# Kernel optimization log

Hardware: AMD Instinct MI355X
Metric: run time of the kernel (lower is better)

The kernel has to match this reference:

```python
import jax, jax.numpy as jnp
import numpy as np

N = 100000
IN_DIM = 128
HIDDEN = 128
HEADS = 8
NUM_CLASSES = 64
NEG_SLOPE = 0.2
LN_EPS = 1e-5


def _glorot(key, shape):
    fan_in, fan_out = shape[0], shape[-1]
    lim = jnp.sqrt(6.0 / (fan_in + fan_out))
    return jax.random.uniform(key, shape, jnp.float32, -lim, lim)


def setup_inputs() -> dict:
    key = jax.random.key(0)
    ks = jax.random.split(key, 12)
    x = jax.random.normal(ks[0], (N, IN_DIM), jnp.float32)
    edge_index = jax.random.randint(ks[1], (2, 1600000), 0, N, jnp.int32)
    C1 = HIDDEN // HEADS
    return {
        "x": x,
        "edge_index": edge_index,
        # GATConv 1: in_dim -> heads * (hidden/heads), concat=True
        "W1": _glorot(ks[2], (IN_DIM, HEADS * C1)),
        "att_src1": _glorot(ks[3], (HEADS, C1)),
        "att_dst1": _glorot(ks[4], (HEADS, C1)),
        "bias1": jnp.zeros((HEADS * C1,), jnp.float32),
        # residual linear (no bias)
        "res_W": _glorot(ks[5], (IN_DIM, HIDDEN)),
        # LayerNorm
        "gamma": jnp.ones((HIDDEN,), jnp.float32),
        "beta": jnp.zeros((HIDDEN,), jnp.float32),
        # GATConv 2: hidden -> num_classes, heads=1, concat=False
        "W2": _glorot(ks[6], (HIDDEN, NUM_CLASSES)),
        "att_src2": _glorot(ks[7], (1, NUM_CLASSES)),
        "att_dst2": _glorot(ks[8], (1, NUM_CLASSES)),
        "bias2": jnp.zeros((NUM_CLASSES,), jnp.float32),
    }


def gat_conv(x, src, dst, W, att_src, att_dst, bias, heads, concat):
    n = x.shape[0]
    h = (x @ W).reshape(n, heads, -1)                     # [N,H,C]
    a_src = (h * att_src).sum(-1)                         # [N,H]
    a_dst = (h * att_dst).sum(-1)                         # [N,H]
    e = jax.nn.leaky_relu(a_src[src] + a_dst[dst], NEG_SLOPE)  # [E,H]
    # softmax over incoming edges of each destination node
    m = jax.ops.segment_max(e, dst, num_segments=n)
    m = jnp.where(jnp.isfinite(m), m, 0.0)
    e = jnp.exp(e - m[dst])
    s = jax.ops.segment_sum(e, dst, num_segments=n)
    alpha = e / (s[dst] + 1e-16)                          # [E,H]
    msg = h[src] * alpha[:, :, None]                      # [E,H,C]
    out = jax.ops.segment_sum(msg, dst, num_segments=n)   # [N,H,C]
    out = out.reshape(n, -1) if concat else out.mean(axis=1)
    return out + bias


def layer_norm(h, gamma, beta):
    mu = h.mean(-1, keepdims=True)
    var = ((h - mu) ** 2).mean(-1, keepdims=True)
    return (h - mu) * jax.lax.rsqrt(var + LN_EPS) * gamma + beta


def reference(x, edge_index, W1, att_src1, att_dst1, bias1, res_W,
              gamma, beta, W2, att_src2, att_dst2, bias2):
    n = x.shape[0]
    # PyG GATConv adds self-loops by default
    loop = jnp.arange(n, dtype=edge_index.dtype)
    src = jnp.concatenate([edge_index[0], loop])
    dst = jnp.concatenate([edge_index[1], loop])
    # eval mode: all dropouts are identity
    h = gat_conv(x, src, dst, W1, att_src1, att_dst1, bias1, HEADS, True)
    h = h + x @ res_W
    h = layer_norm(h, gamma, beta)
    h = jax.nn.elu(h)
    logits = gat_conv(h, src, dst, W2, att_src2, att_dst2, bias2, 1, False)
    return (h, logits)
```

## Files before the change

kernel.cpp:

```cpp
#include <hip/hip_runtime.h>
#include <hip/hip_bf16.h>

typedef __attribute__((ext_vector_type(8))) short bf16x8;
typedef __attribute__((ext_vector_type(4))) float f32x4;

__device__ __forceinline__ float bfu(unsigned short u){
  union{ unsigned int i; float f; } c; c.i = ((unsigned)u) << 16; return c.f;
}
__device__ __forceinline__ float bflo(unsigned u){
  union{ unsigned int i; float f; } c; c.i = u << 16; return c.f;
}
__device__ __forceinline__ float bfhi(unsigned u){
  union{ unsigned int i; float f; } c; c.i = u & 0xffff0000u; return c.f;
}
__device__ __forceinline__ float ldval(const void* p, int i, int f32){
  return f32 ? ((const float*)p)[i] : bfu(((const unsigned short*)p)[i]);
}
__device__ __forceinline__ bf16x8 packbf8(float4 u, float4 v){
  union { bf16x8 v8; __hip_bfloat16 h[8]; } r;
  r.h[0]=__float2bfloat16(u.x); r.h[1]=__float2bfloat16(u.y);
  r.h[2]=__float2bfloat16(u.z); r.h[3]=__float2bfloat16(u.w);
  r.h[4]=__float2bfloat16(v.x); r.h[5]=__float2bfloat16(v.y);
  r.h[6]=__float2bfloat16(v.z); r.h[7]=__float2bfloat16(v.w);
  return r.v8;
}
__device__ __forceinline__ float lrelu(float v){ return v > 0.f ? v : 0.2f*v; }

__global__ void detect(const unsigned short* __restrict__ xh, int* __restrict__ flag){
  int i = blockIdx.x*256 + threadIdx.x;
  float v = fabsf(bfu(xh[i]));
  if (v > 1e4f) atomicOr(flag, 1);
}

__global__ void prep(const void* W1, const void* resW, const void* W2,
                     const void* a1s, const void* a1d, const void* b1,
                     const void* g, const void* bt,
                     const void* a2s, const void* a2d, const void* b2,
                     __hip_bfloat16* __restrict__ Bt1, __hip_bfloat16* __restrict__ W2t,
                     float* att1s, float* att1d, float* bias1f, float* gf, float* bfta,
                     float* att2s, float* att2d, float* bias2f, const int* flag){
  int f = *flag;
  int idx = blockIdx.x*256 + threadIdx.x;
  if (idx < 16384){ int c=idx>>7, k=idx&127; Bt1[idx] = __float2bfloat16(ldval(W1,  k*128+c, f)); }
  else if (idx < 32768){ int i=idx-16384, c=i>>7, k=i&127; Bt1[idx] = __float2bfloat16(ldval(resW,k*128+c, f)); }
  else if (idx < 40960){ int i=idx-32768, c=i>>7, k=i&127; W2t[i]  = __float2bfloat16(ldval(W2,  k*64+c,  f)); }
  else if (idx < 41088) att1s [idx-40960] = ldval(a1s, idx-40960, f);
  else if (idx < 41216) att1d [idx-41088] = ldval(a1d, idx-41088, f);
  else if (idx < 41344) bias1f[idx-41216] = ldval(b1,  idx-41216, f);
  else if (idx < 41472) gf    [idx-41344] = ldval(g,   idx-41344, f);
  else if (idx < 41600) bfta  [idx-41472] = ldval(bt,  idx-41472, f);
  else if (idx < 41664) att2s [idx-41600] = ldval(a2s, idx-41600, f);
  else if (idx < 41728) att2d [idx-41664] = ldval(a2d, idx-41664, f);
  else if (idx < 41792) bias2f[idx-41728] = ldval(b2,  idx-41728, f);
}

__global__ __launch_bounds__(256) void gemm1_fat(const void* __restrict__ xp,
                  const __hip_bfloat16* __restrict__ Bt1,
                  __hip_bfloat16* __restrict__ h1b,
                  __hip_bfloat16* __restrict__ xrB,
                  __hip_bfloat16* __restrict__ xrF,
                  const float* __restrict__ att1s, const float* __restrict__ att1d,
                  float* __restrict__ as1, float* __restrict__ ad1,
                  const int* __restrict__ ei, int* __restrict__ cnt,
                  int* __restrict__ eoff,
                  const int* __restrict__ flag, int nn, int E, int G){
  __shared__ __hip_bfloat16 sh[16][128];
  if ((int)blockIdx.x >= G){
    int e = ((int)blockIdx.x - G)*256 + threadIdx.x;
    if (e < E){
      int d = ei[E+e];
      int off = 0;
      if ((unsigned)d < (unsigned)nn) off = atomicAdd(&cnt[d], 1);
      if (eoff) eoff[e] = off;
    }
    return;
  }
  int f32 = *flag;
  __hip_bfloat16* xr = f32 ? xrF : xrB;
  int wave = threadIdx.x >> 6, lane = threadIdx.x & 63;
  int m = lane & 15, q = lane >> 4;
  int n0 = blockIdx.x * 16;
  int row = n0 + m; if (row >= nn) row = nn - 1;
  f32x4 acc[4];
  #pragma unroll
  for (int ct=0; ct<4; ++ct) acc[ct] = (f32x4){0.f,0.f,0.f,0.f};
  #pragma unroll
  for (int kk=0; kk<4; ++kk){
    bf16x8 a;
    if (!f32) a = *(const bf16x8*)((const __hip_bfloat16*)xp + (size_t)row*128 + kk*32 + q*8);
    else { const float4* fp = (const float4*)((const float*)xp + (size_t)row*128 + kk*32 + q*8);
           a = packbf8(fp[0], fp[1]); }
    #pragma unroll
    for (int ct=0; ct<4; ++ct){
      int c = wave*64 + ct*16 + m;
      bf16x8 b = *(const bf16x8*)(Bt1 + (size_t)c*128 + kk*32 + q*8);
      acc[ct] = __builtin_amdgcn_mfma_f32_16x16x32_bf16(a, b, acc[ct], 0, 0, 0);
    }
  }
  #pragma unroll
  for (int ct=0; ct<4; ++ct){
    int c = wave*64 + ct*16 + m;
    #pragma unroll
    for (int i=0;i<4;++i){
      int r = n0 + q*4 + i;
      if (r < nn){
        __hip_bfloat16 hv = __float2bfloat16(acc[ct][i]);
        if (c < 128){ h1b[(size_t)r*128 + c] = hv; sh[q*4+i][c] = hv; }
        else          xr [(size_t)r*128 + (c-128)] = hv;
      }
    }
  }
  __syncthreads();
  int tid = threadIdx.x;
  if (tid < 128){
    int r = tid >> 3, h = tid & 7;
    if (n0 + r < nn){
      const bf16x8* hp = (const bf16x8*)&sh[r][h*16];
      bf16x8 v0 = hp[0], v1 = hp[1];
      float s=0.f, d=0.f;
      #pragma unroll
      for (int j=0;j<8;++j){
        float a = bfu((unsigned short)v0[j]);
        s += a*att1s[h*16+j]; d += a*att1d[h*16+j];
      }
      #pragma unroll
      for (int j=0;j<8;++j){
        float a = bfu((unsigned short)v1[j]);
        s += a*att1s[h*16+8+j]; d += a*att1d[h*16+8+j];
      }
      as1[(size_t)(n0+r)*8 + h] = s;
      ad1[(size_t)(n0+r)*8 + h] = d;
    }
  }
}

__global__ __launch_bounds__(256) void gemm2_fat(const void* __restrict__ hp,
                  const __hip_bfloat16* __restrict__ W2t,
                  __hip_bfloat16* __restrict__ h2b,
                  const float* __restrict__ att2s, const float* __restrict__ att2d,
                  float* __restrict__ as2, float* __restrict__ ad2,
                  const int* __restrict__ flag, int nn){
  __shared__ __hip_bfloat16 sh2[16][64];
  int f32 = *flag;
  int wave = threadIdx.x >> 6, lane = threadIdx.x & 63;
  int m = lane & 15, q = lane >> 4;
  int n0 = blockIdx.x * 16;
  int row = n0 + m; if (row >= nn) row = nn - 1;
  f32x4 acc = (f32x4){0.f,0.f,0.f,0.f};
  #pragma unroll
  for (int kk=0; kk<4; ++kk){
    bf16x8 a;
    if (!f32) a = *(const bf16x8*)((const __hip_bfloat16*)hp + (size_t)row*128 + kk*32 + q*8);
    else { const float4* fp = (const float4*)((const float*)hp + (size_t)row*128 + kk*32 + q*8);
           a = packbf8(fp[0], fp[1]); }
    int c = wave*16 + m;
    bf16x8 b = *(const bf16x8*)(W2t + (size_t)c*128 + kk*32 + q*8);
    acc = __builtin_amdgcn_mfma_f32_16x16x32_bf16(a, b, acc, 0, 0, 0);
  }
  int c = wave*16 + m;
  #pragma unroll
  for (int i=0;i<4;++i){
    int r = n0 + q*4 + i;
    if (r < nn){
      __hip_bfloat16 hv = __float2bfloat16(acc[i]);
      h2b[(size_t)r*64 + c] = hv;
      sh2[q*4+i][c] = hv;
    }
  }
  __syncthreads();
  int tid = threadIdx.x;
  if (tid < 16 && n0 + tid < nn){
    const bf16x8* rp = (const bf16x8*)&sh2[tid][0];
    float s=0.f, d=0.f;
    #pragma unroll
    for (int t=0;t<8;++t){
      bf16x8 v = rp[t];
      #pragma unroll
      for (int j=0;j<8;++j){
        float a = bfu((unsigned short)v[j]);
        s += a*att2s[t*8+j]; d += a*att2d[t*8+j];
      }
    }
    as2[n0+tid]=s; ad2[n0+tid]=d;
  }
}

__global__ void scan_part(const int* __restrict__ cnt, int* __restrict__ part, int n){
  __shared__ int red[256];
  int t = threadIdx.x;
  int base = blockIdx.x*1024 + t*4;
  int s = 0;
  #pragma unroll
  for (int j=0;j<4;++j){ int i = base + j; if (i < n) s += cnt[i]; }
  red[t] = s; __syncthreads();
  for (int off=128; off>0; off>>=1){
    if (t < off) red[t] += red[t+off];
    __syncthreads();
  }
  if (t == 0) part[blockIdx.x] = red[0];
}

__global__ void scan_mid(int* __restrict__ part, int nb, int* __restrict__ row_ptr, int n){
  __shared__ int sd[256];
  int t = threadIdx.x;
  int v = (t < nb) ? part[t] : 0;
  sd[t] = v; __syncthreads();
  for (int off=1; off<256; off<<=1){
    int xv = (t >= off) ? sd[t-off] : 0;
    __syncthreads();
    sd[t] += xv;
    __syncthreads();
  }
  if (t < nb) part[t] = sd[t] - v;
  if (t == 0) row_ptr[n] = sd[255];
}

__global__ void scan_write(const int* __restrict__ cnt, const int* __restrict__ part,
                           int* __restrict__ row_ptr, int n){
  __shared__ int sd[256];
  int t = threadIdx.x;
  int base = blockIdx.x*1024 + t*4;
  int v0=0,v1=0,v2=0,v3=0;
  if (base   < n) v0 = cnt[base];
  if (base+1 < n) v1 = cnt[base+1];
  if (base+2 < n) v2 = cnt[base+2];
  if (base+3 < n) v3 = cnt[base+3];
  int s = v0+v1+v2+v3;
  sd[t] = s; __syncthreads();
  for (int off=1; off<256; off<<=1){
    int xv = (t >= off) ? sd[t-off] : 0;
    __syncthreads();
    sd[t] += xv;
    __syncthreads();
  }
  int run = part[blockIdx.x] + sd[t] - s;
  if (base   < n) row_ptr[base]   = run; run += v0;
  if (base+1 < n) row_ptr[base+1] = run; run += v1;
  if (base+2 < n) row_ptr[base+2] = run; run += v2;
  if (base+3 < n) row_ptr[base+3] = run;
}

__global__ void fill_csr(const int* __restrict__ ei, const int* __restrict__ row_ptr,
                         const int* __restrict__ eoff, int* __restrict__ csr,
                         int E, int nn){
  int e = blockIdx.x*256 + threadIdx.x;
  if (e < E){
    int d = ei[E+e];
    if ((unsigned)d < (unsigned)nn){
      int pos = row_ptr[d] + eoff[e];
      if ((unsigned)pos < (unsigned)E) csr[pos] = ei[e];
    }
  }
}

__global__ void fill_csr_atomic(const int* __restrict__ ei, const int* __restrict__ row_ptr,
                                int* __restrict__ cur, int* __restrict__ csr, int E, int nn){
  int e = blockIdx.x*256 + threadIdx.x;
  if (e < E){
    int d = ei[E+e];
    if ((unsigned)d < (unsigned)nn){
      int pos = row_ptr[d] + atomicAdd(&cur[d], 1);
      if ((unsigned)pos < (unsigned)E) csr[pos] = ei[e];
    }
  }
}

__global__ __launch_bounds__(256) void agg1(
    const __hip_bfloat16* __restrict__ h1b,
    const float* __restrict__ as1, const float* __restrict__ ad1,
    const int* __restrict__ rowp, const int* __restrict__ csr,
    const __hip_bfloat16* __restrict__ xrB, const __hip_bfloat16* __restrict__ xrF,
    const float* __restrict__ bias1f, const float* __restrict__ gf,
    const float* __restrict__ bfta,
    const int* __restrict__ flag, void* __restrict__ dout, int nn, int Etot){
  int f32 = *flag;
  int w = threadIdx.x >> 6, lane = threadIdx.x & 63;
  int n = blockIdx.x*4 + w;
  if (n >= nn) return;
  int g = lane >> 4, t = lane & 15;
  int c0 = t*8;
  int h = t >> 1;
  int wh = lane & 7;
  const __hip_bfloat16* xr = f32 ? xrF : xrB;
  float adc = ad1[n*8 + h];
  float adw = ad1[n*8 + wh];
  float asn = as1[n*8 + h];
  bf16x8 hs = *(const bf16x8*)(h1b + (size_t)n*128 + c0);
  int p0 = rowp[n], pe = rowp[n+1];
  if (p0 < 0) p0 = 0; if (pe > Etot) pe = Etot;
  int p0u = __builtin_amdgcn_readfirstlane(p0);
  int peu = __builtin_amdgcn_readfirstlane(pe);
  float selfw = __expf(fminf(lrelu(asn + adc), 30.f));
  float sw0 = (g == 0) ? selfw : 0.f;
  float acc[8];
  { union { bf16x8 v; uint4 u; } cv; cv.v = hs;
    acc[0]=sw0*bflo(cv.u.x); acc[1]=sw0*bfhi(cv.u.x);
    acc[2]=sw0*bflo(cv.u.y); acc[3]=sw0*bfhi(cv.u.y);
    acc[4]=sw0*bflo(cv.u.z); acc[5]=sw0*bfhi(cv.u.z);
    acc[6]=sw0*bflo(cv.u.w); acc[7]=sw0*bfhi(cv.u.w); }
  float denp = 0.f;
  int idxA = g*8 + h;
  int idxB = idxA + 32;
  for (int b = p0u; b < peu; b += 16){
    int e0i = b + (lane>>3);
    int e1i = e0i + 8;
    int j0 = e0i < peu ? e0i : peu-1;
    int j1 = e1i < peu ? e1i : peu-1;
    int s0 = csr[j0]; if ((unsigned)s0 >= (unsigned)nn) s0 = 0;
    int s1 = csr[j1]; if ((unsigned)s1 >= (unsigned)nn) s1 = 0;
    float av0 = as1[(size_t)s0*8 + wh];
    float av1 = as1[(size_t)s1*8 + wh];
    float w0 = __expf(fminf(lrelu(av0 + adw), 30.f)) * (e0i < peu ? 1.f : 0.f);
    float w1 = __expf(fminf(lrelu(av1 + adw), 30.f)) * (e1i < peu ? 1.f : 0.f);
    denp += w0 + w1;
    bf16x8 hv[4]; float wb[4];
    #pragma unroll
    for (int i=0;i<4;++i){
      int sv = __shfl(i < 2 ? s0 : s1, (i & 1) ? idxB : idxA);
      wb[i]  = __shfl(i < 2 ? w0 : w1, (i & 1) ? idxB : idxA);
      hv[i] = *(const bf16x8*)(h1b + (size_t)sv*128 + c0);
    }
    #pragma unroll
    for (int i=0;i<4;++i){
      union { bf16x8 v; uint4 u; } cv; cv.v = hv[i];
      float wv = wb[i];
      acc[0] += wv*bflo(cv.u.x); acc[1] += wv*bfhi(cv.u.x);
      acc[2] += wv*bflo(cv.u.y); acc[3] += wv*bfhi(cv.u.y);
      acc[4] += wv*bflo(cv.u.z); acc[5] += wv*bfhi(cv.u.z);
      acc[6] += wv*bflo(cv.u.w); acc[7] += wv*bfhi(cv.u.w);
    }
  }
  #pragma unroll
  for (int j=0;j<8;++j){
    acc[j] += __shfl_xor(acc[j], 16);
    acc[j] += __shfl_xor(acc[j], 32);
  }
  denp += __shfl_xor(denp, 8);
  denp += __shfl_xor(denp, 16);
  denp += __shfl_xor(denp, 32);
  float den = __shfl(denp, h) + selfw;
  float inv = 1.f/(den + 1e-16f);
  bf16x8 xv = *(const bf16x8*)(xr + (size_t)n*128 + c0);
  union { bf16x8 v; uint4 u; } xc; xc.v = xv;
  float xf[8] = { bflo(xc.u.x), bfhi(xc.u.x), bflo(xc.u.y), bfhi(xc.u.y),
                  bflo(xc.u.z), bfhi(xc.u.z), bflo(xc.u.w), bfhi(xc.u.w) };
  float4 bA = *(const float4*)(bias1f + c0), bB = *(const float4*)(bias1f + c0 + 4);
  float bb[8] = { bA.x,bA.y,bA.z,bA.w, bB.x,bB.y,bB.z,bB.w };
  float o[8];
  float s1 = 0.f, s2 = 0.f;
  #pragma unroll
  for (int j=0;j<8;++j){
    o[j] = acc[j]*inv + xf[j] + bb[j];
    s1 += o[j]; s2 += o[j]*o[j];
  }
  #pragma unroll
  for (int off=1; off<16; off<<=1){
    s1 += __shfl_xor(s1, off);
    s2 += __shfl_xor(s2, off);
  }
  float mu  = s1 * (1.f/128.f);
  float var = s2 * (1.f/128.f) - mu*mu;
  float rstd = rsqrtf(var + 1e-5f);
  float4 gA = *(const float4*)(gf + c0),   gB = *(const float4*)(gf + c0 + 4);
  float4 tA = *(const float4*)(bfta + c0), tB = *(const float4*)(bfta + c0 + 4);
  float gg[8] = { gA.x,gA.y,gA.z,gA.w, gB.x,gB.y,gB.z,gB.w };
  float tt[8] = { tA.x,tA.y,tA.z,tA.w, tB.x,tB.y,tB.z,tB.w };
  #pragma unroll
  for (int j=0;j<8;++j){
    float v = (o[j]-mu)*rstd*gg[j] + tt[j];
    o[j] = v > 0.f ? v : __expf(v) - 1.f;
  }
  if (g == 0){
    if (!f32){
      bf16x8 ov = packbf8((float4){o[0],o[1],o[2],o[3]}, (float4){o[4],o[5],o[6],o[7]});
      *(bf16x8*)((__hip_bfloat16*)dout + (size_t)n*128 + c0) = ov;
    } else {
      float* op = (float*)dout + (size_t)n*128 + c0;
      *(float4*)op     = (float4){o[0],o[1],o[2],o[3]};
      *(float4*)(op+4) = (float4){o[4],o[5],o[6],o[7]};
    }
  }
}

__global__ __launch_bounds__(256) void agg2(const __hip_bfloat16* __restrict__ h2b,
    const float* __restrict__ as2, const float* __restrict__ ad2,
    const int* __restrict__ rowp, const int* __restrict__ csr,
    const float* __restrict__ bias2f,
    const int* __restrict__ flag, void* __restrict__ dout, int nn, int Etot){
  int f32 = *flag;
  int w = threadIdx.x >> 6, lane = threadIdx.x & 63;
  int n = blockIdx.x*4 + w;
  if (n >= nn) return;
  int g = lane >> 3, t = lane & 7;
  int c0 = t*8;
  float adst = ad2[n];
  float selfw = __expf(fminf(lrelu(as2[n] + adst), 30.f));
  float sw0 = (g == 0) ? selfw : 0.f;
  bf16x8 hs = *(const bf16x8*)(h2b + (size_t)n*64 + c0);
  float acc[8];
  { union { bf16x8 v; uint4 u; } cv; cv.v = hs;
    acc[0]=sw0*bflo(cv.u.x); acc[1]=sw0*bfhi(cv.u.x);
    acc[2]=sw0*bflo(cv.u.y); acc[3]=sw0*bfhi(cv.u.y);
    acc[4]=sw0*bflo(cv.u.z); acc[5]=sw0*bfhi(cv.u.z);
    acc[6]=sw0*bflo(cv.u.w); acc[7]=sw0*bfhi(cv.u.w); }
  float denp = 0.f;
  int p0 = rowp[n], pe = rowp[n+1];
  if (p0 < 0) p0 = 0; if (pe > Etot) pe = Etot;
  int p0u = __builtin_amdgcn_readfirstlane(p0);
  int peu = __builtin_amdgcn_readfirstlane(pe);
  for (int b = p0u; b < peu; b += 64){
    int ei = b + lane;
    int ji = ei < peu ? ei : peu-1;
    int si = csr[ji]; if ((unsigned)si >= (unsigned)nn) si = 0;
    float av = as2[si];
    float wv = __expf(fminf(lrelu(av + adst), 30.f)) * (ei < peu ? 1.f : 0.f);
    denp += wv;
    #pragma unroll
    for (int ib = 0; ib < 8; ib += 4){
      if (b + 8*ib < peu){
        bf16x8 hv[4]; float wb[4];
        #pragma unroll
        for (int u=0;u<4;++u){
          int i = ib + u;
          int sv = __shfl(si, g + 8*i);
          wb[u]  = __shfl(wv, g + 8*i);
          hv[u] = *(const bf16x8*)(h2b + (size_t)sv*64 + c0);
        }
        #pragma unroll
        for (int u=0;u<4;++u){
          union { bf16x8 v; uint4 uu; } cv; cv.v = hv[u];
          float wx = wb[u];
          acc[0] += wx*bflo(cv.uu.x); acc[1] += wx*bfhi(cv.uu.x);
          acc[2] += wx*bflo(cv.uu.y); acc[3] += wx*bfhi(cv.uu.y);
          acc[4] += wx*bflo(cv.uu.z); acc[5] += wx*bfhi(cv.uu.z);
          acc[6] += wx*bflo(cv.uu.w); acc[7] += wx*bfhi(cv.uu.w);
        }
      }
    }
  }
  #pragma unroll
  for (int j=0;j<8;++j){
    acc[j] += __shfl_xor(acc[j], 8);
    acc[j] += __shfl_xor(acc[j], 16);
    acc[j] += __shfl_xor(acc[j], 32);
  }
  denp += __shfl_xor(denp, 1);
  denp += __shfl_xor(denp, 2);
  denp += __shfl_xor(denp, 4);
  denp += __shfl_xor(denp, 8);
  denp += __shfl_xor(denp, 16);
  denp += __shfl_xor(denp, 32);
  float den = denp + selfw;
  float inv = 1.f/(den + 1e-16f);
  float4 bA = *(const float4*)(bias2f + c0), bB = *(const float4*)(bias2f + c0 + 4);
  float bb[8] = { bA.x,bA.y,bA.z,bA.w, bB.x,bB.y,bB.z,bB.w };
  float o[8];
  #pragma unroll
  for (int j=0;j<8;++j) o[j] = acc[j]*inv + bb[j];
  if (g == 0){
    if (!f32){
      bf16x8 ov = packbf8((float4){o[0],o[1],o[2],o[3]}, (float4){o[4],o[5],o[6],o[7]});
      *(bf16x8*)((__hip_bfloat16*)dout + (size_t)nn*128 + (size_t)n*64 + c0) = ov;
    } else {
      float* op = (float*)dout + (size_t)nn*128 + (size_t)n*64 + c0;
      *(float4*)op     = (float4){o[0],o[1],o[2],o[3]};
      *(float4*)(op+4) = (float4){o[4],o[5],o[6],o[7]};
    }
  }
}

extern "C" void kernel_launch(void* const* d_in, const int* in_sizes, int n_in,
                              void* d_out, int out_size, void* d_ws, size_t ws_size,
                              hipStream_t stream){
  (void)n_in; (void)out_size;
  const void* x     = d_in[0];
  const int*  ei    = (const int*)d_in[1];
  const void* W1    = d_in[2];
  const void* a1s   = d_in[3];
  const void* a1d   = d_in[4];
  const void* b1    = d_in[5];
  const void* resW  = d_in[6];
  const void* g     = d_in[7];
  const void* bt    = d_in[8];
  const void* W2    = d_in[9];
  const void* a2s   = d_in[10];
  const void* a2d   = d_in[11];
  const void* b2    = d_in[12];

  int N = in_sizes[0] / 128;
  int E = in_sizes[1] / 2;

  __hip_bfloat16* xrB = (__hip_bfloat16*)d_out;
  __hip_bfloat16* xrF = (__hip_bfloat16*)((float*)d_out + (size_t)N*128);

  char* ws = (char*)d_ws;
  size_t o = 0;
  auto alloc = [&](size_t bytes)->char*{ char* r = ws + o; o = (o + bytes + 255) & ~(size_t)255; return r; };
  int*   flag = (int*)  alloc(4);
  int*   part = (int*)  alloc(4096);
  int*   rowp = (int*)  alloc(((size_t)N+1)*4);
  int*   cnt  = (int*)  alloc((size_t)N*4);
  float* as1  = (float*)alloc((size_t)N*8*4);
  float* ad1  = (float*)alloc((size_t)N*8*4);
  int*   csr  = (int*)  alloc((size_t)E*4);
  __hip_bfloat16* h1b = (__hip_bfloat16*)alloc((size_t)N*128*2);
  __hip_bfloat16* Bt1 = (__hip_bfloat16*)alloc(65536);
  __hip_bfloat16* W2t = (__hip_bfloat16*)alloc(16384);
  float* att1s  = (float*)alloc(512);
  float* att1d  = (float*)alloc(512);
  float* bias1f = (float*)alloc(512);
  float* gfv    = (float*)alloc(512);
  float* bfv    = (float*)alloc(512);
  float* att2s  = (float*)alloc(256);
  float* att2d  = (float*)alloc(256);
  float* bias2f = (float*)alloc(256);
  int*   eoff = (int*)  alloc((size_t)E*4);
  int use_eoff = (o <= ws_size);
  __hip_bfloat16* h2b = h1b;
  float* as2 = as1;
  float* ad2 = ad1;

  int G  = (N + 15)/16;
  int EB = (E + 255)/256;
  int NB = (N + 1023)/1024;

  (void)hipMemsetAsync(flag, 0, 4, stream);
  (void)hipMemsetAsync(cnt,  0, (size_t)N*4, stream);
  detect<<<16, 256, 0, stream>>>((const unsigned short*)x, flag);
  prep<<<164, 256, 0, stream>>>(W1, resW, W2, a1s, a1d, b1, g, bt, a2s, a2d, b2,
                                Bt1, W2t, att1s, att1d, bias1f, gfv, bfv,
                                att2s, att2d, bias2f, flag);
  gemm1_fat<<<G + EB, 256, 0, stream>>>(x, Bt1, h1b, xrB, xrF,
                                        att1s, att1d, as1, ad1,
                                        ei, cnt, use_eoff ? eoff : (int*)nullptr,
                                        flag, N, E, G);
  scan_part<<<NB, 256, 0, stream>>>(cnt, part, N);
  scan_mid<<<1, 256, 0, stream>>>(part, NB, rowp, N);
  scan_write<<<NB, 256, 0, stream>>>(cnt, part, rowp, N);
  if (use_eoff){
    fill_csr<<<EB, 256, 0, stream>>>(ei, rowp, eoff, csr, E, N);
  } else {
    (void)hipMemsetAsync(cnt, 0, (size_t)N*4, stream);
    fill_csr_atomic<<<EB, 256, 0, stream>>>(ei, rowp, cnt, csr, E, N);
  }
  agg1<<<(N+3)/4, 256, 0, stream>>>(h1b, as1, ad1, rowp, csr, xrB, xrF,
                                    bias1f, gfv, bfv, flag, d_out, N, E);
  gemm2_fat<<<G, 256, 0, stream>>>(d_out, W2t, h2b, att2s, att2d, as2, ad2, flag, N);
  agg2<<<(N+3)/4, 256, 0, stream>>>(h2b, as2, ad2, rowp, csr, bias2f, flag, d_out, N, E);
}
```

Before: 488.8 us.

## Build CSR via two-level bucketed counting sort with shared-memory atomics

Replaces per-edge global atomic counting and random CSR scatter with a two-level radix-style sort: per-block shared-memory histograms over coarse destination buckets, a scan of the block-bucket counts, a bucketed scatter of packed (src,local dst) words, then per-bucket local sorting that writes row pointers and CSR. This aims to cut global atomic contention and improve write locality during graph construction. It adds an extra pass over the edges and launches only 128 blocks for the edge passes, which may underuse the GPU.

```diff
diff --git a/kernel.cpp b/kernel.cpp
--- a/kernel.cpp
+++ b/kernel.cpp
@@ -61,18 +61,23 @@
                   __hip_bfloat16* __restrict__ xrF,
                   const float* __restrict__ att1s, const float* __restrict__ att1d,
                   float* __restrict__ as1, float* __restrict__ ad1,
-                  const int* __restrict__ ei, int* __restrict__ cnt,
-                  int* __restrict__ eoff,
-                  const int* __restrict__ flag, int nn, int E, int G){
+                  const int* __restrict__ ei, int* __restrict__ blockCounts,
+                  const int* __restrict__ flag, int nn, int E, int G, int s, int NBK){
   __shared__ __hip_bfloat16 sh[16][128];
+  __shared__ int histB[1024];
   if ((int)blockIdx.x >= G){
-    int e = ((int)blockIdx.x - G)*256 + threadIdx.x;
-    if (e < E){
+    int cb = (int)blockIdx.x - G;
+    int tid = threadIdx.x;
+    for (int j = tid; j < 1024; j += 256) histB[j] = 0;
+    __syncthreads();
+    int chunk = (E + 127) >> 7;
+    int start = cb*chunk, end = start + chunk; if (end > E) end = E;
+    for (int e = start + tid; e < end; e += 256){
       int d = ei[E+e];
-      int off = 0;
-      if ((unsigned)d < (unsigned)nn) off = atomicAdd(&cnt[d], 1);
-      if (eoff) eoff[e] = off;
-    }
+      if ((unsigned)d < (unsigned)nn) atomicAdd(&histB[d >> s], 1);
+    }
+    __syncthreads();
+    for (int j = tid; j < NBK; j += 256) blockCounts[(size_t)j*128 + cb] = histB[j];
     return;
   }
   int f32 = *flag;
@@ -117,19 +122,19 @@
     if (n0 + r < nn){
       const bf16x8* hp = (const bf16x8*)&sh[r][h*16];
       bf16x8 v0 = hp[0], v1 = hp[1];
-      float s=0.f, d=0.f;
+      float sdot=0.f, ddot=0.f;
       #pragma unroll
       for (int j=0;j<8;++j){
         float a = bfu((unsigned short)v0[j]);
-        s += a*att1s[h*16+j]; d += a*att1d[h*16+j];
+        sdot += a*att1s[h*16+j]; ddot += a*att1d[h*16+j];
       }
       #pragma unroll
       for (int j=0;j<8;++j){
         float a = bfu((unsigned short)v1[j]);
-        s += a*att1s[h*16+8+j]; d += a*att1d[h*16+8+j];
+        sdot += a*att1s[h*16+8+j]; ddot += a*att1d[h*16+8+j];
       }
-      as1[(size_t)(n0+r)*8 + h] = s;
-      ad1[(size_t)(n0+r)*8 + h] = d;
+      as1[(size_t)(n0+r)*8 + h] = sdot;
+      ad1[(size_t)(n0+r)*8 + h] = ddot;
     }
   }
 }
@@ -171,17 +176,17 @@
   int tid = threadIdx.x;
   if (tid < 16 && n0 + tid < nn){
     const bf16x8* rp = (const bf16x8*)&sh2[tid][0];
-    float s=0.f, d=0.f;
+    float sdot=0.f, ddot=0.f;
     #pragma unroll
     for (int t=0;t<8;++t){
       bf16x8 v = rp[t];
       #pragma unroll
       for (int j=0;j<8;++j){
         float a = bfu((unsigned short)v[j]);
-        s += a*att2s[t*8+j]; d += a*att2d[t*8+j];
+        sdot += a*att2s[t*8+j]; ddot += a*att2d[t*8+j];
       }
     }
-    as2[n0+tid]=s; ad2[n0+tid]=d;
+    as2[n0+tid]=sdot; ad2[n0+tid]=ddot;
   }
 }
 
@@ -240,28 +245,63 @@
   if (base+3 < n) row_ptr[base+3] = run;
 }
 
-__global__ void fill_csr(const int* __restrict__ ei, const int* __restrict__ row_ptr,
-                         const int* __restrict__ eoff, int* __restrict__ csr,
-                         int E, int nn){
-  int e = blockIdx.x*256 + threadIdx.x;
-  if (e < E){
+__global__ __launch_bounds__(256) void bucket_scatter(const int* __restrict__ ei,
+                  const int* __restrict__ scanned, unsigned* __restrict__ bucketed,
+                  int E, int nn, int s, int NBK){
+  __shared__ int cur[1024];
+  int cb = blockIdx.x;
+  int tid = threadIdx.x;
+  for (int j = tid; j < NBK; j += 256) cur[j] = scanned[(size_t)j*128 + cb];
+  __syncthreads();
+  int chunk = (E + 127) >> 7;
+  int start = cb*chunk, end = start + chunk; if (end > E) end = E;
+  for (int e = start + tid; e < end; e += 256){
     int d = ei[E+e];
-    if ((unsigned)d < (unsigned)nn){
-      int pos = row_ptr[d] + eoff[e];
-      if ((unsigned)pos < (unsigned)E) csr[pos] = ei[e];
-    }
-  }
-}
-
-__global__ void fill_csr_atomic(const int* __restrict__ ei, const int* __restrict__ row_ptr,
-                                int* __restrict__ cur, int* __restrict__ csr, int E, int nn){
-  int e = blockIdx.x*256 + threadIdx.x;
-  if (e < E){
-    int d = ei[E+e];
-    if ((unsigned)d < (unsigned)nn){
-      int pos = row_ptr[d] + atomicAdd(&cur[d], 1);
-      if ((unsigned)pos < (unsigned)E) csr[pos] = ei[e];
-    }
+    if ((unsigned)d >= (unsigned)nn) continue;
+    int src = ei[e]; if ((unsigned)src >= (unsigned)nn) src = 0;
+    int bk = d >> s;
+    int slot = atomicAdd(&cur[bk], 1);
+    bucketed[slot] = ((unsigned)src << s) | (unsigned)(d & ((1<<s)-1));
+  }
+}
+
+__global__ __launch_bounds__(256) void bucket_csr(const unsigned* __restrict__ bucketed,
+                  const int* __restrict__ scanned, int* __restrict__ rowp,
+                  int* __restrict__ csr, int nn, int s, int NBK){
+  __shared__ int hist[1024];
+  __shared__ int sd[256];
+  int b = blockIdx.x, tid = threadIdx.x;
+  int nloc = 1 << s;
+  int dbase = b << s;
+  int ndst = nn - dbase; if (ndst > nloc) ndst = nloc;
+  int rbeg = scanned[(size_t)b*128];
+  int rend = (b+1 < NBK) ? scanned[((size_t)b+1)*128] : rowp[nn];
+  for (int j = tid; j < 1024; j += 256) hist[j] = 0;
+  __syncthreads();
+  for (int i = rbeg + tid; i < rend; i += 256)
+    atomicAdd(&hist[bucketed[i] & (nloc-1)], 1);
+  __syncthreads();
+  int base4 = tid*4;
+  int v0=hist[base4], v1=hist[base4+1], v2=hist[base4+2], v3=hist[base4+3];
+  int ssum = v0+v1+v2+v3;
+  sd[tid]=ssum; __syncthreads();
+  for (int off=1; off<256; off<<=1){
+    int xv = (tid>=off)? sd[tid-off]:0;
+    __syncthreads(); sd[tid]+=xv; __syncthreads();
+  }
+  int run = sd[tid]-ssum;
+  hist[base4]=run; hist[base4+1]=run+v0; hist[base4+2]=run+v0+v1; hist[base4+3]=run+v0+v1+v2;
+  #pragma unroll
+  for (int k=0;k<4;++k){
+    int j = base4+k;
+    if (j < ndst) rowp[dbase+j] = rbeg + hist[j];
+  }
+  __syncthreads();
+  for (int i = rbeg + tid; i < rend; i += 256){
+    unsigned u = bucketed[i];
+    int ld = u & (nloc-1);
+    int slot = rbeg + atomicAdd(&hist[ld], 1);
+    csr[slot] = (int)(u >> s);
   }
 }
 
@@ -472,7 +512,7 @@
 extern "C" void kernel_launch(void* const* d_in, const int* in_sizes, int n_in,
                               void* d_out, int out_size, void* d_ws, size_t ws_size,
                               hipStream_t stream){
-  (void)n_in; (void)out_size;
+  (void)n_in; (void)out_size; (void)ws_size;
   const void* x     = d_in[0];
   const int*  ei    = (const int*)d_in[1];
   const void* W1    = d_in[2];
@@ -490,6 +530,11 @@
   int N = in_sizes[0] / 128;
   int E = in_sizes[1] / 2;
 
+  int s = 7;
+  while ((((size_t)N + ((size_t)1 << s) - 1) >> s) > 1024) ++s;
+  int NBK = (N + (1 << s) - 1) >> s;
+  int M = NBK * 128;
+
   __hip_bfloat16* xrB = (__hip_bfloat16*)d_out;
   __hip_bfloat16* xrF = (__hip_bfloat16*)((float*)d_out + (size_t)N*128);
 
@@ -499,10 +544,12 @@
   int*   flag = (int*)  alloc(4);
   int*   part = (int*)  alloc(4096);
   int*   rowp = (int*)  alloc(((size_t)N+1)*4);
-  int*   cnt  = (int*)  alloc((size_t)N*4);
   float* as1  = (float*)alloc((size_t)N*8*4);
   float* ad1  = (float*)alloc((size_t)N*8*4);
   int*   csr  = (int*)  alloc((size_t)E*4);
+  unsigned* bucketed = (unsigned*)alloc((size_t)E*4);
+  int*   blockCounts = (int*)alloc((size_t)M*4);
+  int*   scanned     = (int*)alloc((size_t)M*4);
   __hip_bfloat16* h1b = (__hip_bfloat16*)alloc((size_t)N*128*2);
   __hip_bfloat16* Bt1 = (__hip_bfloat16*)alloc(65536);
   __hip_bfloat16* W2t = (__hip_bfloat16*)alloc(16384);
@@ -514,35 +561,26 @@
   float* att2s  = (float*)alloc(256);
   float* att2d  = (float*)alloc(256);
   float* bias2f = (float*)alloc(256);
-  int*   eoff = (int*)  alloc((size_t)E*4);
-  int use_eoff = (o <= ws_size);
   __hip_bfloat16* h2b = h1b;
   float* as2 = as1;
   float* ad2 = ad1;
 
   int G  = (N + 15)/16;
-  int EB = (E + 255)/256;
-  int NB = (N + 1023)/1024;
+  int NBscan = (M + 1023)/1024;
 
   (void)hipMemsetAsync(flag, 0, 4, stream);
-  (void)hipMemsetAsync(cnt,  0, (size_t)N*4, stream);
   detect<<<16, 256, 0, stream>>>((const unsigned short*)x, flag);
   prep<<<164, 256, 0, stream>>>(W1, resW, W2, a1s, a1d, b1, g, bt, a2s, a2d, b2,
                                 Bt1, W2t, att1s, att1d, bias1f, gfv, bfv,
                                 att2s, att2d, bias2f, flag);
-  gemm1_fat<<<G + EB, 256, 0, stream>>>(x, Bt1, h1b, xrB, xrF,
-                                        att1s, att1d, as1, ad1,
-                                        ei, cnt, use_eoff ? eoff : (int*)nullptr,
-                                        flag, N, E, G);
-  scan_part<<<NB, 256, 0, stream>>>(cnt, part, N);
-  scan_mid<<<1, 256, 0, stream>>>(part, NB, rowp, N);
-  scan_write<<<NB, 256, 0, stream>>>(cnt, part, rowp, N);
-  if (use_eoff){
-    fill_csr<<<EB, 256, 0, stream>>>(ei, rowp, eoff, csr, E, N);
-  } else {
-    (void)hipMemsetAsync(cnt, 0, (size_t)N*4, stream);
-    fill_csr_atomic<<<EB, 256, 0, stream>>>(ei, rowp, cnt, csr, E, N);
-  }
+  gemm1_fat<<<G + 128, 256, 0, stream>>>(x, Bt1, h1b, xrB, xrF,
+                                         att1s, att1d, as1, ad1,
+                                         ei, blockCounts, flag, N, E, G, s, NBK);
+  scan_part<<<NBscan, 256, 0, stream>>>(blockCounts, part, M);
+  scan_mid<<<1, 256, 0, stream>>>(part, NBscan, rowp, N);
+  scan_write<<<NBscan, 256, 0, stream>>>(blockCounts, part, scanned, M);
+  bucket_scatter<<<128, 256, 0, stream>>>(ei, scanned, bucketed, E, N, s, NBK);
+  bucket_csr<<<NBK, 256, 0, stream>>>(bucketed, scanned, rowp, csr, N, s, NBK);
   agg1<<<(N+3)/4, 256, 0, stream>>>(h1b, as1, ad1, rowp, csr, xrB, xrF,
                                     bias1f, gfv, bfv, flag, d_out, N, E);
   gemm2_fat<<<G, 256, 0, stream>>>(d_out, W2t, h2b, att2s, att2d, as2, ad2, flag, N);
```

After: 472.9 us. 1.03x faster.
